# Kernel optimization log

Measured on AMD Instinct MI355X. Metric: run time of the kernel, lower is better.

## Reference

```python
import jax, jax.numpy as jnp
import numpy as np

HIDDEN = 128
GATF = 128
HEADS = 4
N_M, N_D = 8192, 6144
N = N_M + N_D


def gcn_conv(x, edges, ew, W, b):
    """PyG GCNConv with edge weights and self-loops (weight 1)."""
    n = x.shape[0]
    loop = jnp.arange(n, dtype=edges.dtype)
    src = jnp.concatenate([edges[0], loop])
    dst = jnp.concatenate([edges[1], loop])
    w = jnp.concatenate([ew, jnp.ones((n,), x.dtype)])
    deg = jax.ops.segment_sum(w, dst, num_segments=n)
    dinv = jnp.where(deg > 0, jax.lax.rsqrt(deg), 0.0)
    norm = dinv[src] * w * dinv[dst]                 # [E+n]
    h = x @ W                                        # [n, F]
    msg = h[src] * norm[:, None]                     # gather + scale
    return jax.ops.segment_sum(msg, dst, num_segments=n) + b


def gatv2_conv(x, edge_index, Wl, Wr, att, bias):
    """PyG GATv2Conv, concat=False (head mean), self-loops, slope 0.2."""
    n = x.shape[0]
    H, C = att.shape
    loop = jnp.arange(n, dtype=edge_index.dtype)
    src = jnp.concatenate([edge_index[0], loop])
    dst = jnp.concatenate([edge_index[1], loop])
    xl = (x @ Wl).reshape(n, H, C)
    xr = (x @ Wr).reshape(n, H, C)
    e = jax.nn.leaky_relu(xl[src] + xr[dst], 0.2)    # [E, H, C]
    logits = jnp.einsum('ehc,hc->eh', e, att)        # [E, H]
    mx = jax.ops.segment_max(logits, dst, num_segments=n)
    ex = jnp.exp(logits - mx[dst])
    denom = jax.ops.segment_sum(ex, dst, num_segments=n)
    alpha = ex / denom[dst]                          # segment softmax
    out = jax.ops.segment_sum(xl[src] * alpha[:, :, None], dst, num_segments=n)
    return out.mean(axis=1) + bias


def setup_inputs() -> dict:
    key = jax.random.key(0)
    ks = jax.random.split(key, 24)
    f32 = jnp.float32
    def glorot(k, shape):
        fan = shape[0] + shape[-1] if len(shape) == 2 else int(np.prod(shape))
        s = np.sqrt(2.0 / fan).astype(np.float32)
        return jax.random.normal(k, shape, f32) * s
    inp = {
        'mm_f': jax.random.normal(ks[0], (N_M, HIDDEN), f32),
        'd_s_feat': jax.random.normal(ks[1], (N_D, HIDDEN), f32),
        'ms_mat': jax.random.uniform(ks[2], (N_M, N_M), f32),
        'ds_mat': jax.random.uniform(ks[3], (N_D, N_D), f32),
        'mm_edges': jax.random.randint(ks[4], (2, 131072), 0, N_M, jnp.int32),
        'dd_edges': jax.random.randint(ks[5], (2, 98304), 0, N_D, jnp.int32),
        'edge_index': jax.random.randint(ks[6], (2, 229376), 0, N, jnp.int32),
        # GCN params
        'W_m1': glorot(ks[7], (HIDDEN, HIDDEN)), 'b_m1': jnp.zeros((HIDDEN,), f32),
        'W_m2': glorot(ks[8], (HIDDEN, HIDDEN)), 'b_m2': jnp.zeros((HIDDEN,), f32),
        'W_d1': glorot(ks[9], (HIDDEN, HIDDEN)), 'b_d1': jnp.zeros((HIDDEN,), f32),
        'W_d2': glorot(ks[10], (HIDDEN, HIDDEN)), 'b_d2': jnp.zeros((HIDDEN,), f32),
        # GATv2 layer 1: GATF -> GATF//2 per head, HEADS heads
        'Wl1': glorot(ks[11], (GATF, HEADS * (GATF // 2))),
        'Wr1': glorot(ks[12], (GATF, HEADS * (GATF // 2))),
        'att1': glorot(ks[13], (HEADS, GATF // 2)),
        'bias1': jnp.zeros((GATF // 2,), f32),
        # GATv2 layer 2: GATF//2 -> GATF//4 per head
        'Wl2': glorot(ks[14], (GATF // 2, HEADS * (GATF // 4))),
        'Wr2': glorot(ks[15], (GATF // 2, HEADS * (GATF // 4))),
        'att2': glorot(ks[16], (HEADS, GATF // 4)),
        'bias2': jnp.zeros((GATF // 4,), f32),
        # JK linear: (GATF + GATF//2 + GATF//4) -> HIDDEN
        'W_jk': glorot(ks[17], (GATF + GATF // 2 + GATF // 4, HIDDEN)),
        'b_jk': jnp.zeros((HIDDEN,), f32),
    }
    return inp


def reference(mm_f, d_s_feat, ms_mat, ds_mat, mm_edges, dd_edges, edge_index,
              W_m1, b_m1, W_m2, b_m2, W_d1, b_d1, W_d2, b_d2,
              Wl1, Wr1, att1, bias1, Wl2, Wr2, att2, bias2, W_jk, b_jk):
    # GCN_GAT feature extraction
    ew_m = ms_mat[mm_edges[0], mm_edges[1]]
    ew_d = ds_mat[dd_edges[0], dd_edges[1]]
    m1 = jax.nn.relu(gcn_conv(mm_f, mm_edges, ew_m, W_m1, b_m1))
    m2 = gcn_conv(m1, mm_edges, ew_m, W_m2, b_m2)
    d1 = jax.nn.relu(gcn_conv(d_s_feat, dd_edges, ew_d, W_d1, b_d1))
    d2 = gcn_conv(d1, dd_edges, ew_d, W_d2, b_d2)
    x0 = jnp.concatenate([jax.nn.relu(m2), jax.nn.relu(d2)], axis=0)  # [N, GATF]
    # GATv2 stack with JumpingKnowledge('cat')
    x1 = jax.nn.elu(gatv2_conv(x0, edge_index, Wl1, Wr1, att1, bias1))
    x2 = gatv2_conv(x1, edge_index, Wl2, Wr2, att2, bias2)
    xjk = jnp.concatenate([x0, x1, x2], axis=-1)
    return xjk @ W_jk + b_jk
```

## Files before the change

### kernel.cpp

```cpp
#include <hip/hip_runtime.h>
#include <math.h>

#define NM   8192
#define NDD  6144
#define NN   14336
#define EMM  131072
#define EDD  98304
#define E2   (EMM + EDD)
#define EGAT 229376
#define WSEG 176128

typedef __attribute__((ext_vector_type(8))) short bf16x8;
typedef __attribute__((ext_vector_type(4))) float f32x4;

static __device__ __forceinline__ ushort f2bf(float x) {
  unsigned u = __float_as_uint(x);
  unsigned r = (u + 0x7FFFu + ((u >> 16) & 1u)) >> 16;
  return (ushort)r;
}
static __device__ __forceinline__ float bf2f(ushort h) {
  return __uint_as_float(((unsigned)h) << 16);
}
static __device__ __forceinline__ void split_store(float x, ushort* ph, ushort* pl) {
  ushort hh = f2bf(x);
  *ph = hh;
  *pl = f2bf(x - bf2f(hh));
}

__global__ __launch_bounds__(256) void prep_kern(
    float* __restrict__ deg, int* __restrict__ cg, int* __restrict__ ca,
    const float* W0, const float* W1, const float* W2, const float* W3,
    const float* W4, const float* W5, const float* W6, const float* W7,
    const float* W8, ushort* __restrict__ wdst,
    const float* __restrict__ fa, const float* __restrict__ fb,
    ushort* __restrict__ oh, ushort* __restrict__ ol) {
  int idx = blockIdx.x * 256 + threadIdx.x;
  if (idx < NN) { deg[idx] = 1.0f; cg[idx] = 0; ca[idx] = 0; }
  int i1 = idx - NN;
  if (i1 >= 0 && i1 < WSEG) {
    const int cum[9] = {16384, 32768, 49152, 65536, 98304, 131072, 139264, 147456, 176128};
    const int Ks[9]  = {128, 128, 128, 128, 128, 128, 64, 64, 224};
    const int Ns[9]  = {128, 128, 128, 128, 256, 256, 128, 128, 128};
    const float* Ws[9] = {W0, W1, W2, W3, W4, W5, W6, W7, W8};
    int seg = 0;
    while (i1 >= cum[seg]) seg++;
    int base = seg ? cum[seg - 1] : 0;
    int S = cum[seg] - base;
    int o = i1 - base;
    int K = Ks[seg], Nn = Ns[seg];
    int n = o / K, k = o - n * K;
    float x = Ws[seg][(size_t)k * Nn + n];
    split_store(x, wdst + 2 * (size_t)base + o, wdst + 2 * (size_t)base + S + o);
  }
  int i2 = idx - (NN + WSEG);
  if (i2 >= 0 && i2 < NN * 128) {
    float x = (i2 < NM * 128) ? fa[i2] : fb[i2 - NM * 128];
    split_store(x, oh + i2, ol + i2);
  }
}

__global__ __launch_bounds__(256) void hist_kern(
    const float* __restrict__ ms, const float* __restrict__ dsm,
    const int* __restrict__ mmE, const int* __restrict__ ddE,
    const int* __restrict__ eidx,
    float* __restrict__ ew, float* __restrict__ deg,
    int* __restrict__ cnt_gcn, int* __restrict__ cnt_gat) {
  int e = blockIdx.x * 256 + threadIdx.x;
  if (e < E2) {
    float w; int dg;
    if (e < EMM) {
      int s = mmE[e], d = mmE[EMM + e];
      w = ms[(size_t)s * NM + d]; dg = d;
    } else {
      int e2 = e - EMM;
      int s = ddE[e2], d = ddE[EDD + e2];
      w = dsm[(size_t)s * NDD + d]; dg = d + NM;
    }
    ew[e] = w;
    atomicAdd(deg + dg, w);
    atomicAdd(cnt_gcn + dg, 1);
  } else {
    int e2 = e - E2;
    if (e2 < EGAT) atomicAdd(cnt_gat + eidx[EGAT + e2], 1);
  }
}

__global__ __launch_bounds__(1024) void scan_kern(
    const int* __restrict__ cntA, int* rsA, int* curA,
    const int* __restrict__ cntB, int* rsB, int* curB,
    float* __restrict__ deg) {
  const int* cnt = blockIdx.x ? cntB : cntA;
  int* rs  = blockIdx.x ? rsB : rsA;
  int* cur = blockIdx.x ? curB : curA;
  for (int i = threadIdx.x; i < NN / 2; i += 1024) {
    int j = blockIdx.x * (NN / 2) + i;
    deg[j] = 1.0f / sqrtf(deg[j]);
  }
  __shared__ int wsum[16];
  __shared__ int carry_s;
  int t = threadIdx.x, w = t >> 6, lane = t & 63;
  if (t == 0) carry_s = 0;
  __syncthreads();
  for (int base = 0; base < NN; base += 1024) {
    int v = cnt[base + t];
    int inc = v;
#pragma unroll
    for (int off = 1; off < 64; off <<= 1) {
      int x = __shfl_up(inc, off);
      if (lane >= off) inc += x;
    }
    if (lane == 63) wsum[w] = inc;
    __syncthreads();
    int carry = carry_s;
    if (w == 0 && lane < 16) {
      int s = wsum[lane];
#pragma unroll
      for (int off = 1; off < 16; off <<= 1) {
        int x = __shfl_up(s, off);
        if (lane >= off) s += x;
      }
      wsum[lane] = s;
    }
    __syncthreads();
    int woff = w ? wsum[w - 1] : 0;
    int excl = carry + woff + inc - v;
    rs[base + t] = excl;
    cur[base + t] = excl;
    if (t == 0) carry_s = carry + wsum[15];
    __syncthreads();
  }
  if (threadIdx.x == 0) rs[NN] = carry_s;
}

__global__ __launch_bounds__(256) void fill_kern(
    const int* __restrict__ mmE, const int* __restrict__ ddE,
    const int* __restrict__ eidx,
    const float* __restrict__ ew, const float* __restrict__ dinv,
    int* __restrict__ cur_gcn, int* __restrict__ csrc, float* __restrict__ cw,
    int* __restrict__ cur_gat, int* __restrict__ gsrc) {
  int e = blockIdx.x * 256 + threadIdx.x;
  if (e < E2) {
    int sg, dg;
    if (e < EMM) { sg = mmE[e]; dg = mmE[EMM + e]; }
    else { int e2 = e - EMM; sg = ddE[e2] + NM; dg = ddE[EDD + e2] + NM; }
    float nrm = dinv[sg] * ew[e] * dinv[dg];
    int pos = atomicAdd(cur_gcn + dg, 1);
    csrc[pos] = sg; cw[pos] = nrm;
  } else {
    int e2 = e - E2;
    if (e2 < EGAT) {
      int src = eidx[e2], dst = eidx[EGAT + e2];
      int pos = atomicAdd(cur_gat + dst, 1);
      gsrc[pos] = src;
    }
  }
}

template <int KT, int NT, bool BIAS, bool DUAL>
__global__ __launch_bounds__(256) void gemm_kern(
    const ushort* __restrict__ Ah, const ushort* __restrict__ Al,
    int lda, int aoff,
    const ushort* __restrict__ WhA, const ushort* __restrict__ WlA,
    const ushort* __restrict__ WhB, const ushort* __restrict__ WlB,
    int splitRow,
    const float* __restrict__ bias,
    float* __restrict__ Ca, float* __restrict__ Cb, int ldc) {
  constexpr int NS = KT / 32;
  int w = threadIdx.x >> 6, lane = threadIdx.x & 63;
  int m0 = blockIdx.x * 64 + w * 16;
  const ushort* Wh; const ushort* Wl; float* C;
  if (DUAL) {
    Wh = blockIdx.y ? WhB : WhA;
    Wl = blockIdx.y ? WlB : WlA;
    C  = blockIdx.y ? Cb : Ca;
  } else {
    Wh = (m0 < splitRow) ? WhA : WhB;
    Wl = (m0 < splitRow) ? WlA : WlB;
    C  = Ca;
  }
  int lm = lane & 15, kg = lane >> 4;
  bf16x8 ah[NS], al[NS];
  const ushort* ap = Ah + (size_t)(m0 + lm) * lda + aoff + kg * 8;
  const ushort* aq = Al + (size_t)(m0 + lm) * lda + aoff + kg * 8;
#pragma unroll
  for (int s = 0; s < NS; s++) {
    ah[s] = *reinterpret_cast<const bf16x8*>(ap + s * 32);
    al[s] = *reinterpret_cast<const bf16x8*>(aq + s * 32);
  }
#pragma unroll
  for (int nb = 0; nb < NT / 16; nb++) {
    int n0 = nb * 16;
    const ushort* wp = Wh + (size_t)(n0 + lm) * KT + kg * 8;
    const ushort* wq = Wl + (size_t)(n0 + lm) * KT + kg * 8;
    f32x4 acc = {0.f, 0.f, 0.f, 0.f};
#pragma unroll
    for (int s = 0; s < NS; s++) {
      bf16x8 wh = *reinterpret_cast<const bf16x8*>(wp + s * 32);
      bf16x8 wl = *reinterpret_cast<const bf16x8*>(wq + s * 32);
      acc = __builtin_amdgcn_mfma_f32_16x16x32_bf16(ah[s], wh, acc, 0, 0, 0);
      acc = __builtin_amdgcn_mfma_f32_16x16x32_bf16(al[s], wh, acc, 0, 0, 0);
      acc = __builtin_amdgcn_mfma_f32_16x16x32_bf16(ah[s], wl, acc, 0, 0, 0);
    }
#pragma unroll
    for (int r = 0; r < 4; r++) {
      float v = acc[r];
      if (BIAS) v += bias[n0 + lm];
      C[(size_t)(m0 + kg * 4 + r) * ldc + n0 + lm] = v;
    }
  }
}

__global__ __launch_bounds__(256) void gcn_gather_kern(
    const float* __restrict__ h, const float* __restrict__ dinv,
    const float* __restrict__ ba, const float* __restrict__ bb,
    const int* __restrict__ rs, const int* __restrict__ csrc,
    const float* __restrict__ cw,
    ushort* __restrict__ outh, ushort* __restrict__ outl, int ldo) {
  int n = blockIdx.x * 2 + (threadIdx.x >> 7);
  int f = threadIdx.x & 127;
  float di = dinv[n];
  const float* b = (n < NM) ? ba : bb;
  float acc = b[f] + h[(size_t)n * 128 + f] * di * di;
  int p = rs[n], p1 = rs[n + 1];
  for (; p + 1 < p1; p += 2) {
    int s0 = csrc[p], s1 = csrc[p + 1];
    float w0 = cw[p], w1 = cw[p + 1];
    acc += h[(size_t)s0 * 128 + f] * w0;
    acc += h[(size_t)s1 * 128 + f] * w1;
  }
  if (p < p1) acc += h[(size_t)csrc[p] * 128 + f] * cw[p];
  acc = fmaxf(acc, 0.f);
  size_t o = (size_t)n * ldo + f;
  split_store(acc, outh + o, outl + o);
}

template <int C, bool ELU>
__global__ __launch_bounds__(4 * C) void gat_gather_kern(
    const float* __restrict__ xl, const float* __restrict__ xr,
    const float* __restrict__ att, const float* __restrict__ bias,
    const int* __restrict__ rs, const int* __restrict__ gsrc,
    ushort* __restrict__ outh, ushort* __restrict__ outl, int ldo, int off) {
  constexpr int HC = 4 * C;
  constexpr int VPL = C / 16;
  constexpr int WAVES = HC / 64;
  __shared__ float xr_s[HC], att_s[HC];
  __shared__ float aws[WAVES][HC];
  __shared__ float mws[WAVES][4], dws[WAVES][4];
  int n = blockIdx.x;
  int tid = threadIdx.x, w = tid >> 6, lane = tid & 63;
  xr_s[tid] = xr[(size_t)n * HC + tid];
  att_s[tid] = att[tid];
  int p0 = rs[n];
  int deg = rs[n + 1] - p0;
  int tot = deg + 1;
  __syncthreads();
  int h0 = lane >> 4;
  float xrv[VPL], atv[VPL];
#pragma unroll
  for (int v = 0; v < VPL; v++) {
    xrv[v] = xr_s[lane * VPL + v];
    atv[v] = att_s[lane * VPL + v];
  }
  float m = -1e30f, d = 0.f, a[VPL];
#pragma unroll
  for (int v = 0; v < VPL; v++) a[v] = 0.f;
  for (int ee = w; ee < tot; ee += WAVES) {
    int src = (ee < deg) ? gsrc[p0 + ee] : n;
    const float* xlr = xl + (size_t)src * HC + lane * VPL;
    float xv[VPL];
    if constexpr (VPL == 4) {
      float4 t4 = *reinterpret_cast<const float4*>(xlr);
      xv[0] = t4.x; xv[1] = t4.y; xv[2] = t4.z; xv[3] = t4.w;
    } else {
      float2 t2 = *reinterpret_cast<const float2*>(xlr);
      xv[0] = t2.x; xv[1] = t2.y;
    }
    float s = 0.f;
#pragma unroll
    for (int v = 0; v < VPL; v++) {
      float t = xv[v] + xrv[v];
      t = (t > 0.f) ? t : 0.2f * t;
      s += t * atv[v];
    }
    s += __shfl_xor(s, 1); s += __shfl_xor(s, 2);
    s += __shfl_xor(s, 4); s += __shfl_xor(s, 8);
    float mn = fmaxf(m, s);
    float cs = __expf(m - mn);
    float ps = __expf(s - mn);
    d = d * cs + ps;
#pragma unroll
    for (int v = 0; v < VPL; v++) a[v] = a[v] * cs + ps * xv[v];
    m = mn;
  }
#pragma unroll
  for (int v = 0; v < VPL; v++) aws[w][lane * VPL + v] = a[v];
  if ((lane & 15) == 0) { mws[w][h0] = m; dws[w][h0] = d; }
  __syncthreads();
  int hh = tid / C;
  float M = mws[0][hh];
#pragma unroll
  for (int w2 = 1; w2 < WAVES; w2++) M = fmaxf(M, mws[w2][hh]);
  float D = 0.f, A = 0.f;
#pragma unroll
  for (int w2 = 0; w2 < WAVES; w2++) {
    float sc = __expf(mws[w2][hh] - M);
    D += dws[w2][hh] * sc;
    A += aws[w2][tid] * sc;
  }
  float sum = A / D;
  __syncthreads();
  aws[0][tid] = sum;
  __syncthreads();
  if (tid < C) {
    float vv = 0.25f * (aws[0][tid] + aws[0][C + tid] +
                        aws[0][2 * C + tid] + aws[0][3 * C + tid]) + bias[tid];
    if (ELU) vv = (vv > 0.f) ? vv : (__expf(vv) - 1.f);
    size_t o = (size_t)n * ldo + off + tid;
    split_store(vv, outh + o, outl + o);
  }
}

extern "C" void kernel_launch(void* const* d_in, const int* in_sizes, int n_in,
                              void* d_out, int out_size, void* d_ws, size_t ws_size,
                              hipStream_t stream) {
  const float* mm_f = (const float*)d_in[0];
  const float* d_sf = (const float*)d_in[1];
  const float* msM  = (const float*)d_in[2];
  const float* dsM  = (const float*)d_in[3];
  const int*   mmE  = (const int*)d_in[4];
  const int*   ddE  = (const int*)d_in[5];
  const int*   eidx = (const int*)d_in[6];
  const float* W_m1 = (const float*)d_in[7];  const float* b_m1 = (const float*)d_in[8];
  const float* W_m2 = (const float*)d_in[9];  const float* b_m2 = (const float*)d_in[10];
  const float* W_d1 = (const float*)d_in[11]; const float* b_d1 = (const float*)d_in[12];
  const float* W_d2 = (const float*)d_in[13]; const float* b_d2 = (const float*)d_in[14];
  const float* Wl1  = (const float*)d_in[15]; const float* Wr1  = (const float*)d_in[16];
  const float* att1 = (const float*)d_in[17]; const float* bias1= (const float*)d_in[18];
  const float* Wl2  = (const float*)d_in[19]; const float* Wr2  = (const float*)d_in[20];
  const float* att2 = (const float*)d_in[21]; const float* bias2= (const float*)d_in[22];
  const float* W_jk = (const float*)d_in[23]; const float* b_jk = (const float*)d_in[24];
  float* out = (float*)d_out;

  float* ew   = (float*)d_ws;
  float* cw   = ew + E2;
  float* dinv = cw + E2;
  float* h    = dinv + NN;
  float* xl   = h + (size_t)NN * 128;
  float* xr   = xl + (size_t)NN * 256;
  ushort* us   = (ushort*)(xr + (size_t)NN * 256);
  ushort* inh  = us;
  ushort* inl  = inh + (size_t)NN * 128;
  ushort* m1h  = inl + (size_t)NN * 128;
  ushort* m1l  = m1h + (size_t)NN * 128;
  ushort* xjkh = m1l + (size_t)NN * 128;
  ushort* xjkl = xjkh + (size_t)NN * 224;
  ushort* wts  = xjkl + (size_t)NN * 224;
  int* ip      = (int*)(wts + 352256);
  int* cnt_gcn = ip;
  int* rs_gcn  = cnt_gcn + NN;
  int* cur_gcn = rs_gcn + NN + 1;
  int* cnt_gat = cur_gcn + NN;
  int* rs_gat  = cnt_gat + NN;
  int* cur_gat = rs_gat + NN + 1;
  int* csrc    = cur_gat + NN;
  int* gsrc    = csrc + E2;

  ushort* m1Wh = wts + 0;      ushort* m1Wl = wts + 16384;
  ushort* m2Wh = wts + 32768;  ushort* m2Wl = wts + 49152;
  ushort* d1Wh = wts + 65536;  ushort* d1Wl = wts + 81920;
  ushort* d2Wh = wts + 98304;  ushort* d2Wl = wts + 114688;
  ushort* l1Wh = wts + 131072; ushort* l1Wl = wts + 163840;
  ushort* r1Wh = wts + 196608; ushort* r1Wl = wts + 229376;
  ushort* l2Wh = wts + 262144; ushort* l2Wl = wts + 270336;
  ushort* r2Wh = wts + 278528; ushort* r2Wl = wts + 286720;
  ushort* jkWh = wts + 294912; ushort* jkWl = wts + 323584;

  const int BIG = 1 << 30;

  prep_kern<<<(NN + WSEG + NN * 128) / 256, 256, 0, stream>>>(
      dinv, cnt_gcn, cnt_gat,
      W_m1, W_m2, W_d1, W_d2, Wl1, Wr1, Wl2, Wr2, W_jk, wts,
      mm_f, d_sf, inh, inl);
  hist_kern<<<(E2 + EGAT) / 256, 256, 0, stream>>>(
      msM, dsM, mmE, ddE, eidx, ew, dinv, cnt_gcn, cnt_gat);
  scan_kern<<<2, 1024, 0, stream>>>(cnt_gcn, rs_gcn, cur_gcn,
                                    cnt_gat, rs_gat, cur_gat, dinv);
  fill_kern<<<(E2 + EGAT) / 256, 256, 0, stream>>>(
      mmE, ddE, eidx, ew, dinv, cur_gcn, csrc, cw, cur_gat, gsrc);

  gemm_kern<128, 128, false, false><<<dim3(NN / 64, 1), 256, 0, stream>>>(
      inh, inl, 128, 0, m1Wh, m1Wl, d1Wh, d1Wl, NM, nullptr, h, nullptr, 128);
  gcn_gather_kern<<<NN / 2, 256, 0, stream>>>(
      h, dinv, b_m1, b_d1, rs_gcn, csrc, cw, m1h, m1l, 128);

  gemm_kern<128, 128, false, false><<<dim3(NN / 64, 1), 256, 0, stream>>>(
      m1h, m1l, 128, 0, m2Wh, m2Wl, d2Wh, d2Wl, NM, nullptr, h, nullptr, 128);
  gcn_gather_kern<<<NN / 2, 256, 0, stream>>>(
      h, dinv, b_m2, b_d2, rs_gcn, csrc, cw, xjkh, xjkl, 224);

  gemm_kern<128, 256, false, true><<<dim3(NN / 64, 2), 256, 0, stream>>>(
      xjkh, xjkl, 224, 0, l1Wh, l1Wl, r1Wh, r1Wl, 0, nullptr, xl, xr, 256);
  gat_gather_kern<64, true><<<NN, 256, 0, stream>>>(
      xl, xr, att1, bias1, rs_gat, gsrc, xjkh, xjkl, 224, 128);

  gemm_kern<64, 128, false, true><<<dim3(NN / 64, 2), 256, 0, stream>>>(
      xjkh, xjkl, 224, 128, l2Wh, l2Wl, r2Wh, r2Wl, 0, nullptr, xl, xr, 128);
  gat_gather_kern<32, false><<<NN, 128, 0, stream>>>(
      xl, xr, att2, bias2, rs_gat, gsrc, xjkh, xjkl, 224, 192);

  gemm_kern<224, 128, true, false><<<dim3(NN / 64, 1), 256, 0, stream>>>(
      xjkh, xjkl, 224, 0, jkWh, jkWl, jkWh, jkWl, BIG, b_jk, out, nullptr, 128);
}
```

Before: 695.1 us.

## Store GAT xl in bf16, split GEMM N across blocks, unroll gathers

The GATv2 source projection xl is now written as bf16 instead of fp32, which halves the bytes moved by the per-edge gathers in the attention kernels. The attention kernel processes two edges per wave iteration to get more loads in flight. The GCN gather unrolls by four, and every GEMM splits its output columns across a second grid dimension for more parallelism. The cost is lower precision in xl, which feeds both the attention logits and the aggregated messages, so the result may drift from the fp32 reference.

Result: faster. 661.2 us (-4.9%).

```diff
diff --git a/kernel.cpp b/kernel.cpp
--- a/kernel.cpp
+++ b/kernel.cpp
@@ -25,6 +25,10 @@
   ushort hh = f2bf(x);
   *ph = hh;
   *pl = f2bf(x - bf2f(hh));
+}
+static __device__ __forceinline__ void unpack2(unsigned u, float& a, float& b) {
+  a = __uint_as_float((u & 0xFFFFu) << 16);
+  b = __uint_as_float(u & 0xFFFF0000u);
 }
 
 __global__ __launch_bounds__(256) void prep_kern(
@@ -156,7 +160,7 @@
   }
 }
 
-template <int KT, int NT, bool BIAS, bool DUAL>
+template <int KT, int NT, int NSPLIT, bool BIAS, bool DUAL>
 __global__ __launch_bounds__(256) void gemm_kern(
     const ushort* __restrict__ Ah, const ushort* __restrict__ Al,
     int lda, int aoff,
@@ -164,20 +168,14 @@
     const ushort* __restrict__ WhB, const ushort* __restrict__ WlB,
     int splitRow,
     const float* __restrict__ bias,
-    float* __restrict__ Ca, float* __restrict__ Cb, int ldc) {
+    void* __restrict__ Ca, void* __restrict__ Cb, int ldc) {
   constexpr int NS = KT / 32;
+  constexpr int NBP = (NT / 16) / NSPLIT;
   int w = threadIdx.x >> 6, lane = threadIdx.x & 63;
   int m0 = blockIdx.x * 64 + w * 16;
-  const ushort* Wh; const ushort* Wl; float* C;
-  if (DUAL) {
-    Wh = blockIdx.y ? WhB : WhA;
-    Wl = blockIdx.y ? WlB : WlA;
-    C  = blockIdx.y ? Cb : Ca;
-  } else {
-    Wh = (m0 < splitRow) ? WhA : WhB;
-    Wl = (m0 < splitRow) ? WlA : WlB;
-    C  = Ca;
-  }
+  bool isA = DUAL ? (blockIdx.z == 0) : (m0 < splitRow);
+  const ushort* Wh = isA ? WhA : WhB;
+  const ushort* Wl = isA ? WlA : WlB;
   int lm = lane & 15, kg = lane >> 4;
   bf16x8 ah[NS], al[NS];
   const ushort* ap = Ah + (size_t)(m0 + lm) * lda + aoff + kg * 8;
@@ -188,8 +186,8 @@
     al[s] = *reinterpret_cast<const bf16x8*>(aq + s * 32);
   }
 #pragma unroll
-  for (int nb = 0; nb < NT / 16; nb++) {
-    int n0 = nb * 16;
+  for (int nb = 0; nb < NBP; nb++) {
+    int n0 = (blockIdx.y * NBP + nb) * 16;
     const ushort* wp = Wh + (size_t)(n0 + lm) * KT + kg * 8;
     const ushort* wq = Wl + (size_t)(n0 + lm) * KT + kg * 8;
     f32x4 acc = {0.f, 0.f, 0.f, 0.f};
@@ -205,7 +203,10 @@
     for (int r = 0; r < 4; r++) {
       float v = acc[r];
       if (BIAS) v += bias[n0 + lm];
-      C[(size_t)(m0 + kg * 4 + r) * ldc + n0 + lm] = v;
+      size_t o = (size_t)(m0 + kg * 4 + r) * ldc + n0 + lm;
+      if (DUAL && blockIdx.z == 0) ((ushort*)Ca)[o] = f2bf(v);
+      else if (DUAL) ((float*)Cb)[o] = v;
+      else ((float*)Ca)[o] = v;
     }
   }
 }
@@ -222,13 +223,16 @@
   const float* b = (n < NM) ? ba : bb;
   float acc = b[f] + h[(size_t)n * 128 + f] * di * di;
   int p = rs[n], p1 = rs[n + 1];
-  for (; p + 1 < p1; p += 2) {
-    int s0 = csrc[p], s1 = csrc[p + 1];
-    float w0 = cw[p], w1 = cw[p + 1];
-    acc += h[(size_t)s0 * 128 + f] * w0;
-    acc += h[(size_t)s1 * 128 + f] * w1;
-  }
-  if (p < p1) acc += h[(size_t)csrc[p] * 128 + f] * cw[p];
+  for (; p + 3 < p1; p += 4) {
+    int s0 = csrc[p], s1 = csrc[p + 1], s2 = csrc[p + 2], s3 = csrc[p + 3];
+    float w0 = cw[p], w1 = cw[p + 1], w2 = cw[p + 2], w3 = cw[p + 3];
+    float h0 = h[(size_t)s0 * 128 + f];
+    float h1 = h[(size_t)s1 * 128 + f];
+    float h2 = h[(size_t)s2 * 128 + f];
+    float h3 = h[(size_t)s3 * 128 + f];
+    acc += h0 * w0 + h1 * w1 + h2 * w2 + h3 * w3;
+  }
+  for (; p < p1; p++) acc += h[(size_t)csrc[p] * 128 + f] * cw[p];
   acc = fmaxf(acc, 0.f);
   size_t o = (size_t)n * ldo + f;
   split_store(acc, outh + o, outl + o);
@@ -236,7 +240,7 @@
 
 template <int C, bool ELU>
 __global__ __launch_bounds__(4 * C) void gat_gather_kern(
-    const float* __restrict__ xl, const float* __restrict__ xr,
+    const ushort* __restrict__ xl, const float* __restrict__ xr,
     const float* __restrict__ att, const float* __restrict__ bias,
     const int* __restrict__ rs, const int* __restrict__ gsrc,
     ushort* __restrict__ outh, ushort* __restrict__ outl, int ldo, int off) {
@@ -264,32 +268,45 @@
   float m = -1e30f, d = 0.f, a[VPL];
 #pragma unroll
   for (int v = 0; v < VPL; v++) a[v] = 0.f;
-  for (int ee = w; ee < tot; ee += WAVES) {
-    int src = (ee < deg) ? gsrc[p0 + ee] : n;
-    const float* xlr = xl + (size_t)src * HC + lane * VPL;
-    float xv[VPL];
+  for (int ee = w; ee < tot; ee += 2 * WAVES) {
+    int e1 = ee + WAVES;
+    bool has2 = (e1 < tot);
+    int src0 = (ee < deg) ? gsrc[p0 + ee] : n;
+    int src1 = has2 ? ((e1 < deg) ? gsrc[p0 + e1] : n) : src0;
+    float xv0[VPL], xv1[VPL];
     if constexpr (VPL == 4) {
-      float4 t4 = *reinterpret_cast<const float4*>(xlr);
-      xv[0] = t4.x; xv[1] = t4.y; xv[2] = t4.z; xv[3] = t4.w;
+      uint2 r0 = *reinterpret_cast<const uint2*>(xl + (size_t)src0 * HC + lane * 4);
+      uint2 r1 = *reinterpret_cast<const uint2*>(xl + (size_t)src1 * HC + lane * 4);
+      unpack2(r0.x, xv0[0], xv0[1]); unpack2(r0.y, xv0[2], xv0[3]);
+      unpack2(r1.x, xv1[0], xv1[1]); unpack2(r1.y, xv1[2], xv1[3]);
     } else {
-      float2 t2 = *reinterpret_cast<const float2*>(xlr);
-      xv[0] = t2.x; xv[1] = t2.y;
-    }
-    float s = 0.f;
+      unsigned r0 = *reinterpret_cast<const unsigned*>(xl + (size_t)src0 * HC + lane * 2);
+      unsigned r1 = *reinterpret_cast<const unsigned*>(xl + (size_t)src1 * HC + lane * 2);
+      unpack2(r0, xv0[0], xv0[1]);
+      unpack2(r1, xv1[0], xv1[1]);
+    }
+    float s0 = 0.f, s1 = 0.f;
 #pragma unroll
     for (int v = 0; v < VPL; v++) {
-      float t = xv[v] + xrv[v];
-      t = (t > 0.f) ? t : 0.2f * t;
-      s += t * atv[v];
-    }
-    s += __shfl_xor(s, 1); s += __shfl_xor(s, 2);
-    s += __shfl_xor(s, 4); s += __shfl_xor(s, 8);
-    float mn = fmaxf(m, s);
+      float t0 = xv0[v] + xrv[v];
+      t0 = (t0 > 0.f) ? t0 : 0.2f * t0;
+      s0 += t0 * atv[v];
+      float t1 = xv1[v] + xrv[v];
+      t1 = (t1 > 0.f) ? t1 : 0.2f * t1;
+      s1 += t1 * atv[v];
+    }
+    s0 += __shfl_xor(s0, 1); s0 += __shfl_xor(s0, 2);
+    s0 += __shfl_xor(s0, 4); s0 += __shfl_xor(s0, 8);
+    s1 += __shfl_xor(s1, 1); s1 += __shfl_xor(s1, 2);
+    s1 += __shfl_xor(s1, 4); s1 += __shfl_xor(s1, 8);
+    if (!has2) s1 = -1e30f;
+    float mn = fmaxf(m, fmaxf(s0, s1));
     float cs = __expf(m - mn);
-    float ps = __expf(s - mn);
-    d = d * cs + ps;
-#pragma unroll
-    for (int v = 0; v < VPL; v++) a[v] = a[v] * cs + ps * xv[v];
+    float q0 = __expf(s0 - mn);
+    float q1 = __expf(s1 - mn);
+    d = d * cs + q0 + q1;
+#pragma unroll
+    for (int v = 0; v < VPL; v++) a[v] = a[v] * cs + q0 * xv0[v] + q1 * xv1[v];
     m = mn;
   }
 #pragma unroll
@@ -345,10 +362,10 @@
   float* cw   = ew + E2;
   float* dinv = cw + E2;
   float* h    = dinv + NN;
-  float* xl   = h + (size_t)NN * 128;
-  float* xr   = xl + (size_t)NN * 256;
+  float* xr   = h + (size_t)NN * 128;
   ushort* us   = (ushort*)(xr + (size_t)NN * 256);
-  ushort* inh  = us;
+  ushort* xlb  = us;
+  ushort* inh  = xlb + (size_t)NN * 256;
   ushort* inl  = inh + (size_t)NN * 128;
   ushort* m1h  = inl + (size_t)NN * 128;
   ushort* m1l  = m1h + (size_t)NN * 128;
@@ -388,26 +405,26 @@
   fill_kern<<<(E2 + EGAT) / 256, 256, 0, stream>>>(
       mmE, ddE, eidx, ew, dinv, cur_gcn, csrc, cw, cur_gat, gsrc);
 
-  gemm_kern<128, 128, false, false><<<dim3(NN / 64, 1), 256, 0, stream>>>(
+  gemm_kern<128, 128, 2, false, false><<<dim3(NN / 64, 2, 1), 256, 0, stream>>>(
       inh, inl, 128, 0, m1Wh, m1Wl, d1Wh, d1Wl, NM, nullptr, h, nullptr, 128);
   gcn_gather_kern<<<NN / 2, 256, 0, stream>>>(
       h, dinv, b_m1, b_d1, rs_gcn, csrc, cw, m1h, m1l, 128);
 
-  gemm_kern<128, 128, false, false><<<dim3(NN / 64, 1), 256, 0, stream>>>(
+  gemm_kern<128, 128, 2, false, false><<<dim3(NN / 64, 2, 1), 256, 0, stream>>>(
       m1h, m1l, 128, 0, m2Wh, m2Wl, d2Wh, d2Wl, NM, nullptr, h, nullptr, 128);
   gcn_gather_kern<<<NN / 2, 256, 0, stream>>>(
       h, dinv, b_m2, b_d2, rs_gcn, csrc, cw, xjkh, xjkl, 224);
 
-  gemm_kern<128, 256, false, true><<<dim3(NN / 64, 2), 256, 0, stream>>>(
-      xjkh, xjkl, 224, 0, l1Wh, l1Wl, r1Wh, r1Wl, 0, nullptr, xl, xr, 256);
+  gemm_kern<128, 256, 2, false, true><<<dim3(NN / 64, 2, 2), 256, 0, stream>>>(
+      xjkh, xjkl, 224, 0, l1Wh, l1Wl, r1Wh, r1Wl, 0, nullptr, xlb, xr, 256);
   gat_gather_kern<64, true><<<NN, 256, 0, stream>>>(
-      xl, xr, att1, bias1, rs_gat, gsrc, xjkh, xjkl, 224, 128);
-
-  gemm_kern<64, 128, false, true><<<dim3(NN / 64, 2), 256, 0, stream>>>(
-      xjkh, xjkl, 224, 128, l2Wh, l2Wl, r2Wh, r2Wl, 0, nullptr, xl, xr, 128);
+      xlb, xr, att1, bias1, rs_gat, gsrc, xjkh, xjkl, 224, 128);
+
+  gemm_kern<64, 128, 2, false, true><<<dim3(NN / 64, 2, 2), 256, 0, stream>>>(
+      xjkh, xjkl, 224, 128, l2Wh, l2Wl, r2Wh, r2Wl, 0, nullptr, xlb, xr, 128);
   gat_gather_kern<32, false><<<NN, 128, 0, stream>>>(
-      xl, xr, att2, bias2, rs_gat, gsrc, xjkh, xjkl, 224, 192);
-
-  gemm_kern<224, 128, true, false><<<dim3(NN / 64, 1), 256, 0, stream>>>(
+      xlb, xr, att2, bias2, rs_gat, gsrc, xjkh, xjkl, 224, 192);
+
+  gemm_kern<224, 128, 2, true, false><<<dim3(NN / 64, 2, 1), 256, 0, stream>>>(
       xjkh, xjkl, 224, 0, jkWh, jkWl, jkWh, jkWl, BIG, b_jk, out, nullptr, 128);
 }
```
